# Kernel tuning notes

Hardware: AMD Instinct MI355X
Metric: run time of the kernel (lower is better)

Reference implementation:

```python
import jax, jax.numpy as jnp
import numpy as np

NUM_FEATURES = 4
LATENT = 16
HIDDEN = 128
N_PIECES = 20
B, P = 8192, 128


def setup_inputs() -> dict:
    key = jax.random.key(0)
    ks = jax.random.split(key, 8)
    s = lambda fan_in: 1.0 / np.sqrt(fan_in)
    return {
        "x": jax.random.normal(ks[0], (B, P * NUM_FEATURES), jnp.float32),
        "W1": jax.random.normal(ks[1], (NUM_FEATURES, HIDDEN), jnp.float32) * s(NUM_FEATURES),
        "b1": jnp.zeros((HIDDEN,), jnp.float32),
        "W2": jax.random.normal(ks[2], (HIDDEN, HIDDEN), jnp.float32) * s(HIDDEN),
        "b2": jnp.zeros((HIDDEN,), jnp.float32),
        "W3": jax.random.normal(ks[3], (HIDDEN, 2 * LATENT), jnp.float32) * s(HIDDEN),
        "b3": jnp.zeros((2 * LATENT,), jnp.float32),
        "pool_weight": jax.random.normal(ks[4], (2 * LATENT, N_PIECES + 1), jnp.float32) * 0.1,
        "eps": jax.random.normal(ks[5], (B, LATENT), jnp.float32),
    }


def _fspool_weights(pool_weight, set_size):
    # piecewise-linear interpolation of pool_weight over normalized rank positions
    pos = jnp.arange(set_size, dtype=jnp.float32) / (set_size - 1) * N_PIECES  # [P]
    idx = jnp.clip(pos.astype(jnp.int32), 0, N_PIECES)
    frac = pos - idx.astype(jnp.float32)
    left = pool_weight[:, idx]                                   # [C, P]
    right = pool_weight[:, jnp.clip(idx + 1, 0, N_PIECES)]       # [C, P]
    return (1.0 - frac) * left + frac * right                    # [C, P]


def reference(x, W1, b1, W2, b2, W3, b3, pool_weight, eps):
    # per-particle shared MLP, batched over particles (B, P, F) -> (B, P, 2L)
    h = x.reshape(B, P, NUM_FEATURES)
    h = jax.nn.relu(jnp.einsum("bpf,fh->bph", h, W1) + b1)
    h = jax.nn.relu(jnp.einsum("bph,hk->bpk", h, W2) + b2)
    h = jnp.einsum("bph,hc->bpc", h, W3) + b3                    # [B, P, 2L]
    z = jnp.transpose(h, (0, 2, 1))                              # [B, 2L, P]
    # FSPool: descending featurewise sort + rank-weighted sum over set dim
    z_sorted = jnp.flip(jnp.sort(z, axis=-1), axis=-1)           # [B, 2L, P]
    w = _fspool_weights(pool_weight, P)                          # [2L, P]
    pooled = jnp.sum(z_sorted * w[None], axis=-1)                # [B, 2L]
    mus = pooled[:, ::2]
    logvars = pooled[:, 1::2]
    samples = mus + eps * jnp.exp(0.5 * logvars)
    return (mus, logvars, samples)
```

## Files before the change

### kernel.cpp

```cpp
#include <hip/hip_runtime.h>

#define B_TOT 8192
#define NB    16
#define NPCS  20

typedef __attribute__((ext_vector_type(8))) __fp16 f16x8;
typedef __attribute__((ext_vector_type(4))) float f32x4;
typedef __attribute__((ext_vector_type(2))) __fp16 fp16x2;

__device__ __forceinline__ unsigned pkmax(unsigned a, unsigned b) {
    unsigned d; asm("v_pk_max_f16 %0, %1, %2" : "=v"(d) : "v"(a), "v"(b)); return d;
}
__device__ __forceinline__ unsigned pkmin(unsigned a, unsigned b) {
    unsigned d; asm("v_pk_min_f16 %0, %1, %2" : "=v"(d) : "v"(a), "v"(b)); return d;
}
__device__ __forceinline__ unsigned pkrne(float a, float b) {
    fp16x2 h;
    h.x = (__fp16)a;
    h.y = (__fp16)b;
    return __builtin_bit_cast(unsigned, h);
}
__device__ __forceinline__ unsigned pkrtz(float a, float b) {
    return __builtin_bit_cast(unsigned, __builtin_amdgcn_cvt_pkrtz(a, b));
}
__device__ __forceinline__ float asf(unsigned u) { return __builtin_bit_cast(float, u); }
__device__ __forceinline__ unsigned asu(float f) { return __builtin_bit_cast(unsigned, f); }
__device__ __forceinline__ fp16x2 ash2(unsigned u) { return __builtin_bit_cast(fp16x2, u); }
__device__ __forceinline__ unsigned asu2(fp16x2 h) { return __builtin_bit_cast(unsigned, h); }

template<int CTRL>
__device__ __forceinline__ unsigned dppmov(unsigned v) {
    return (unsigned)__builtin_amdgcn_mov_dpp((int)v, CTRL, 0xf, 0xf, true);
}
__device__ __forceinline__ unsigned xlane(unsigned v, int lm) {
    switch (lm) {
    case 1:  return dppmov<0xB1>(v);
    case 2:  return dppmov<0x4E>(v);
    case 4:  return (unsigned)__builtin_amdgcn_ds_swizzle((int)v, 0x101F);
    default: return dppmov<0x128>(v);
    }
}
__device__ __forceinline__ float xlanef(float v, int lm) { return asf(xlane(asu(v), lm)); }

#define WS_W3T 32768
#define WS_WSP 40960
#define WS_W1D 57344
#define WS_B1D 59392

__device__ __forceinline__ unsigned dup16(float f) {
    unsigned short u = __builtin_bit_cast(unsigned short, (__fp16)f);
    return (unsigned)u * 0x10001u;
}

__device__ __forceinline__ int piperm(int j) {
    return (j & 0x60) | ((j & 0x0C) << 1) | ((j & 0x10) >> 2) | (j & 3);
}

__global__ void prep_kernel(const float* __restrict__ W1, const float* __restrict__ b1,
                            const float* __restrict__ W2, const float* __restrict__ W3,
                            const float* __restrict__ pw, void* __restrict__ ws)
{
    const int t = blockIdx.x * 256 + threadIdx.x;
    __fp16* w2t = (__fp16*)ws;
    __fp16* w3t = (__fp16*)((char*)ws + WS_W3T);
    float* wsp  = (float*)((char*)ws + WS_WSP);
    unsigned* w1d = (unsigned*)((char*)ws + WS_W1D);
    unsigned* b1d = (unsigned*)((char*)ws + WS_B1D);
    if (t < 16384) {
        int j = t >> 7, k = t & 127;
        w2t[t] = (__fp16)W2[k * 128 + piperm(j)];
    } else if (t < 20480) {
        int o = t - 16384, c = o >> 7, k = o & 127;
        w3t[o] = (__fp16)W3[k * 32 + c];
    } else if (t < 24576) {
        int o = t - 20480, c = o >> 7, p = o & 127;
        float pos = (float)p * (20.0f / 127.0f);
        int ip = min((int)pos, NPCS);
        float fr = pos - (float)ip;
        int ipb = min(ip + 1, NPCS);
        wsp[o] = (1.0f - fr) * pw[c * 21 + ip] + fr * pw[c * 21 + ipb];
    } else if (t < 24704) {
        int h = t - 24576;
        w1d[h * 4 + 0] = dup16(W1[h]);
        w1d[h * 4 + 1] = dup16(W1[128 + h]);
        w1d[h * 4 + 2] = dup16(W1[256 + h]);
        w1d[h * 4 + 3] = dup16(W1[384 + h]);
        b1d[h] = dup16(b1[h]);
    }
}

#define L_SZP  32768
#define L_W1D  41216
#define L_B1D  43264
#define L_POOL 43776

__global__ __launch_bounds__(256, 2) void enc_kernel(
    const float* __restrict__ x,   const float* __restrict__ b1g,
    const float* __restrict__ b2g, const float* __restrict__ b3g,
    const float* __restrict__ eps, const void* __restrict__ ws,
    float* __restrict__ out)
{
    __shared__ __align__(16) char smem[45824];

    const int tid  = threadIdx.x;
    const int wv   = tid >> 6;
    const int lane = tid & 63;
    const int l16  = lane & 15;
    const int quad = lane >> 4;
    const int b0   = blockIdx.x * NB;

    {
        const uint4* src = (const uint4*)ws;
#pragma unroll
        for (int it = 0; it < 8; ++it) {
            int idx = tid + it * 256;
            int j = idx >> 4, ch = idx & 15;
            *(uint4*)(smem + j * 256 + ((ch ^ (j & 15)) * 16)) = src[idx];
        }
    }
    if (tid < 160) ((uint4*)(smem + L_W1D))[tid] = ((const uint4*)((const char*)ws + WS_W1D))[tid];

    f16x8 w3f[2][4];
    {
        const __fp16* w3t = (const __fp16*)((const char*)ws + WS_W3T);
#pragma unroll
        for (int mt2 = 0; mt2 < 2; ++mt2)
#pragma unroll
            for (int kt = 0; kt < 4; ++kt)
                w3f[mt2][kt] = *(const f16x8*)(w3t + (mt2 * 16 + l16) * 128 + kt * 32 + quad * 8);
    }
    f32x4 b3acc[2];
    {
        float4 t0 = *(const float4*)(b3g + quad * 4);
        float4 t1 = *(const float4*)(b3g + 16 + quad * 4);
        b3acc[0] = (f32x4){t0.x, t0.y, t0.z, t0.w};
        b3acc[1] = (f32x4){t1.x, t1.y, t1.z, t1.w};
    }
    f32x4 b2acc[8];
#pragma unroll
    for (int nt = 0; nt < 8; ++nt) {
        float4 t4 = *(const float4*)(b2g + (nt >> 1) * 32 + quad * 8 + (nt & 1) * 4);
        b2acc[nt] = (f32x4){t4.x, t4.y, t4.z, t4.w};
    }

    const int pr = wv * 4 + quad;
    float wE[8], wO[8];
    {
        const float* wsp = (const float*)((const char*)ws + WS_WSP);
        float4 e0 = *(const float4*)(wsp + (2 * pr) * 128 + l16 * 8);
        float4 e1 = *(const float4*)(wsp + (2 * pr) * 128 + l16 * 8 + 4);
        float4 o0 = *(const float4*)(wsp + (2 * pr + 1) * 128 + l16 * 8);
        float4 o1 = *(const float4*)(wsp + (2 * pr + 1) * 128 + l16 * 8 + 4);
        wE[0]=e0.x; wE[1]=e0.y; wE[2]=e0.z; wE[3]=e0.w; wE[4]=e1.x; wE[5]=e1.y; wE[6]=e1.z; wE[7]=e1.w;
        wO[0]=o0.x; wO[1]=o0.y; wO[2]=o0.z; wO[3]=o0.w; wO[4]=o1.x; wO[5]=o1.y; wO[6]=o1.z; wO[7]=o1.w;
    }

    const int ib = l16 * 8;
    const unsigned sfl8  = (ib & 8)  ? 0x80008000u : 0u;
    const unsigned sfl16 = (ib & 16) ? 0x80008000u : 0u;
    const unsigned sfl32 = (ib & 32) ? 0x80008000u : 0u;
    const unsigned sfl64 = (ib & 64) ? 0x80008000u : 0u;

    __syncthreads();

    unsigned* szp   = (unsigned*)(smem + L_SZP);
    float*    spool = (float*)(smem + L_POOL);

    const float* xptr = x + (size_t)b0 * 512 + (wv * 32 + l16) * 4;
    float4 xv0 = *(const float4*)(xptr);
    float4 xv1 = *(const float4*)(xptr + 64);

    for (int e = 0; e < NB; ++e) {
        const unsigned xp0 = pkrtz(xv0.x, xv1.x);
        const unsigned xp1 = pkrtz(xv0.y, xv1.y);
        const unsigned xp2 = pkrtz(xv0.z, xv1.z);
        const unsigned xp3 = pkrtz(xv0.w, xv1.w);

        if (e + 1 < NB) {
            xv0 = *(const float4*)(xptr + (e + 1) * 512);
            xv1 = *(const float4*)(xptr + (e + 1) * 512 + 64);
        }

        union AF { unsigned u[4]; f16x8 v; } a1[2][4];
#pragma unroll
        for (int kt = 0; kt < 4; ++kt) {
            const int k8 = kt * 32 + quad * 8;
#pragma unroll
            for (int jp = 0; jp < 4; ++jp) {
                const int h = k8 + 2 * jp;
                const uint4 wa = *(const uint4*)(smem + L_W1D + h * 16);
                const uint4 wb = *(const uint4*)(smem + L_W1D + h * 16 + 16);
                const uint2 bp = *(const uint2*)(smem + L_B1D + h * 4);
                fp16x2 accA = ash2(bp.x);
                fp16x2 accB = ash2(bp.y);
                accA = __builtin_elementwise_fma(ash2(xp0), ash2(wa.x), accA);
                accA = __builtin_elementwise_fma(ash2(xp1), ash2(wa.y), accA);
                accA = __builtin_elementwise_fma(ash2(xp2), ash2(wa.z), accA);
                accA = __builtin_elementwise_fma(ash2(xp3), ash2(wa.w), accA);
                accB = __builtin_elementwise_fma(ash2(xp0), ash2(wb.x), accB);
                accB = __builtin_elementwise_fma(ash2(xp1), ash2(wb.y), accB);
                accB = __builtin_elementwise_fma(ash2(xp2), ash2(wb.z), accB);
                accB = __builtin_elementwise_fma(ash2(xp3), ash2(wb.w), accB);
                const unsigned uA = pkmax(asu2(accA), 0u);
                const unsigned uB = pkmax(asu2(accB), 0u);
                a1[0][kt].u[jp] = __builtin_amdgcn_perm(uA, uB, 0x01000504u);
                a1[1][kt].u[jp] = __builtin_amdgcn_perm(uA, uB, 0x03020706u);
            }
        }

        f32x4 acc2[2][8];
#pragma unroll
        for (int kt = 0; kt < 4; ++kt)
#pragma unroll
            for (int nt = 0; nt < 8; ++nt) {
                const int j = nt * 16 + l16;
                const int phys = (kt * 4 + quad) ^ l16;
                f16x8 wf = *(const f16x8*)(smem + j * 256 + phys * 16);
                if (kt == 0) {
                    acc2[0][nt] = __builtin_amdgcn_mfma_f32_16x16x32_f16(wf, a1[0][0].v, b2acc[nt], 0, 0, 0);
                    acc2[1][nt] = __builtin_amdgcn_mfma_f32_16x16x32_f16(wf, a1[1][0].v, b2acc[nt], 0, 0, 0);
                } else {
                    acc2[0][nt] = __builtin_amdgcn_mfma_f32_16x16x32_f16(wf, a1[0][kt].v, acc2[0][nt], 0, 0, 0);
                    acc2[1][nt] = __builtin_amdgcn_mfma_f32_16x16x32_f16(wf, a1[1][kt].v, acc2[1][nt], 0, 0, 0);
                }
            }

#pragma unroll
        for (int mt = 0; mt < 2; ++mt) {
            unsigned pkx[8], pky[8];
#pragma unroll
            for (int nt = 0; nt < 8; ++nt) {
                pkx[nt] = pkmax(pkrtz(acc2[mt][nt][0], acc2[mt][nt][1]), 0u);
                pky[nt] = pkmax(pkrtz(acc2[mt][nt][2], acc2[mt][nt][3]), 0u);
            }
            union A3 { unsigned u[4]; f16x8 v; } a3[4];
#pragma unroll
            for (int kt = 0; kt < 4; ++kt) {
                a3[kt].u[0] = pkx[2 * kt];
                a3[kt].u[1] = pky[2 * kt];
                a3[kt].u[2] = pkx[2 * kt + 1];
                a3[kt].u[3] = pky[2 * kt + 1];
            }

            const int colbase = wv * 32 + mt * 16;
#pragma unroll
            for (int mt2 = 0; mt2 < 2; ++mt2) {
                f32x4 acc = __builtin_amdgcn_mfma_f32_16x16x32_f16(w3f[mt2][0], a3[0].v, b3acc[mt2], 0, 0, 0);
#pragma unroll
                for (int kt = 1; kt < 4; ++kt)
                    acc = __builtin_amdgcn_mfma_f32_16x16x32_f16(w3f[mt2][kt], a3[kt].v, acc, 0, 0, 0);
                const int prw = 8 * mt2 + 2 * quad;
                szp[prw * 132 + colbase + l16]       = pkrne(acc[0], acc[1]);
                szp[(prw + 1) * 132 + colbase + l16] = pkrne(acc[2], acc[3]);
            }
        }
        __syncthreads();

        unsigned v[8];
        {
            const unsigned* zp = szp + pr * 132 + l16 * 8;
            uint4 za = *(const uint4*)zp;
            uint4 zb = *(const uint4*)(zp + 4);
            v[0]=za.x; v[1]=za.y; v[2]=za.z; v[3]=za.w;
            v[4]=zb.x; v[5]=zb.y; v[6]=zb.z; v[7]=zb.w;
        }
#pragma unroll
        for (int k = 2; k <= 128; k <<= 1) {
#pragma unroll
            for (int j = 64; j >= 1; j >>= 1) {
                if (j >= k) continue;
                if (j >= 8) {
                    const bool km = ((ib & k) == 0) != ((ib & j) != 0);
                    const int lm = j >> 3;
#pragma unroll
                    for (int r = 0; r < 8; ++r) {
                        unsigned p = xlane(v[r], lm);
                        unsigned mx = pkmax(v[r], p), mn = pkmin(v[r], p);
                        v[r] = km ? mx : mn;
                    }
                } else if (k <= 4) {
#pragma unroll
                    for (int a = 0; a < 8; ++a) {
                        if (a & j) continue;
                        const int bx = a | j;
                        unsigned mx = pkmax(v[a], v[bx]), mn = pkmin(v[a], v[bx]);
                        if ((a & k) == 0) { v[a] = mx; v[bx] = mn; }
                        else              { v[a] = mn; v[bx] = mx; }
                    }
                } else {
                    const unsigned sfl = (k == 8) ? sfl8 : (k == 16) ? sfl16 :
                                         (k == 32) ? sfl32 : (k == 64) ? sfl64 : 0u;
                    if (j == 4 && k != 128) {
#pragma unroll
                        for (int r = 0; r < 8; ++r) v[r] ^= sfl;
                    }
#pragma unroll
                    for (int a = 0; a < 8; ++a) {
                        if (a & j) continue;
                        const int bx = a | j;
                        unsigned mx = pkmax(v[a], v[bx]), mn = pkmin(v[a], v[bx]);
                        v[a] = mx; v[bx] = mn;
                    }
                    if (j == 1 && k != 128) {
#pragma unroll
                        for (int r = 0; r < 8; ++r) v[r] ^= sfl;
                    }
                }
            }
        }

        float sE = 0.f, sO = 0.f;
#pragma unroll
        for (int r = 0; r < 8; ++r) {
            const fp16x2 hv = ash2(v[r]);
            sE = fmaf(wE[r], (float)hv.x, sE);
            sO = fmaf(wO[r], (float)hv.y, sO);
        }
#pragma unroll
        for (int d = 8; d >= 1; d >>= 1) {
            sE += xlanef(sE, d);
            sO += xlanef(sO, d);
        }
        if (l16 == 0) {
            spool[e * 32 + 2 * pr]     = sE;
            spool[e * 32 + 2 * pr + 1] = sO;
        }
        __syncthreads();
    }

    {
        const int e = tid >> 4, t = tid & 15;
        const float mu = spool[e * 32 + 2 * t];
        const float lv = spool[e * 32 + 2 * t + 1];
        const float ev = eps[(size_t)b0 * 16 + tid];
        const float smp = fmaf(ev, __expf(0.5f * lv), mu);
        out[(size_t)b0 * 16 + tid] = mu;
        out[(size_t)B_TOT * 16 + (size_t)b0 * 16 + tid] = lv;
        out[(size_t)2 * B_TOT * 16 + (size_t)b0 * 16 + tid] = smp;
    }
}

extern "C" void kernel_launch(void* const* d_in, const int* in_sizes, int n_in,
                              void* d_out, int out_size, void* d_ws, size_t ws_size,
                              hipStream_t stream) {
    const float* x   = (const float*)d_in[0];
    const float* W1  = (const float*)d_in[1];
    const float* b1  = (const float*)d_in[2];
    const float* W2  = (const float*)d_in[3];
    const float* b2  = (const float*)d_in[4];
    const float* W3  = (const float*)d_in[5];
    const float* b3  = (const float*)d_in[6];
    const float* pw  = (const float*)d_in[7];
    const float* eps = (const float*)d_in[8];
    float* out = (float*)d_out;

    prep_kernel<<<dim3(97), dim3(256), 0, stream>>>(W1, b1, W2, W3, pw, d_ws);
    enc_kernel<<<dim3(B_TOT / NB), dim3(256), 0, stream>>>(x, b1, b2, b3, eps, d_ws, out);
}
```

Measured before the change: 157.6 us.

## Compute first MLP layer with MFMA instead of packed fp16 FMAs

Replaces the per-lane packed-half FMA evaluation of layer 1 (4 inputs to 128 hidden) with 16x16x32 MFMA ops. W1 and b1 are prepacked into register-resident A fragments, with the bias folded in through a constant-one input column. This removes the W1/b1 LDS tables and their per-iteration shared-memory reads and VALU FMAs. In exchange it spends 16 MFMAs per element on mostly zero-padded K, plus extra fp32-to-fp16 conversions and more registers for the W1 fragments.

```diff
diff --git a/kernel.cpp b/kernel.cpp
--- a/kernel.cpp
+++ b/kernel.cpp
@@ -44,12 +44,13 @@
 
 #define WS_W3T 32768
 #define WS_WSP 40960
-#define WS_W1D 57344
-#define WS_B1D 59392
-
-__device__ __forceinline__ unsigned dup16(float f) {
-    unsigned short u = __builtin_bit_cast(unsigned short, (__fp16)f);
-    return (unsigned)u * 0x10001u;
+#define WS_W1A 57344
+#define WS_B1F 61440
+
+__device__ __forceinline__ unsigned packh2(float lo, float hi) {
+    unsigned short a = __builtin_bit_cast(unsigned short, (__fp16)lo);
+    unsigned short b = __builtin_bit_cast(unsigned short, (__fp16)hi);
+    return (unsigned)a | ((unsigned)b << 16);
 }
 
 __device__ __forceinline__ int piperm(int j) {
@@ -64,8 +65,8 @@
     __fp16* w2t = (__fp16*)ws;
     __fp16* w3t = (__fp16*)((char*)ws + WS_W3T);
     float* wsp  = (float*)((char*)ws + WS_WSP);
-    unsigned* w1d = (unsigned*)((char*)ws + WS_W1D);
-    unsigned* b1d = (unsigned*)((char*)ws + WS_B1D);
+    unsigned* w1a = (unsigned*)((char*)ws + WS_W1A);
+    unsigned* b1f = (unsigned*)((char*)ws + WS_B1F);
     if (t < 16384) {
         int j = t >> 7, k = t & 127;
         w2t[t] = (__fp16)W2[k * 128 + piperm(j)];
@@ -79,20 +80,31 @@
         float fr = pos - (float)ip;
         int ipb = min(ip + 1, NPCS);
         wsp[o] = (1.0f - fr) * pw[c * 21 + ip] + fr * pw[c * 21 + ipb];
-    } else if (t < 24704) {
-        int h = t - 24576;
-        w1d[h * 4 + 0] = dup16(W1[h]);
-        w1d[h * 4 + 1] = dup16(W1[128 + h]);
-        w1d[h * 4 + 2] = dup16(W1[256 + h]);
-        w1d[h * 4 + 3] = dup16(W1[384 + h]);
-        b1d[h] = dup16(b1[h]);
+    } else if (t < 25600) {
+        int idx = t - 24576;
+        int ht = idx >> 7, lane = (idx >> 1) & 63, pair = idx & 1;
+        int quad = lane >> 4, l16 = lane & 15;
+        unsigned val = 0;
+        if (quad == 0) {
+            int sh = piperm(16 * ht + l16);
+            val = packh2(W1[(2 * pair) * 128 + sh], W1[(2 * pair + 1) * 128 + sh]);
+        }
+        w1a[idx] = val;
+    } else if (t < 26112) {
+        int idx = t - 25600;
+        int ht = idx >> 6, lane = idx & 63;
+        int quad = lane >> 4, l16 = lane & 15;
+        unsigned val = 0;
+        if (quad == 0) {
+            int sh = piperm(16 * ht + l16);
+            val = packh2(b1[sh], 0.0f);
+        }
+        b1f[idx] = val;
     }
 }
 
 #define L_SZP  32768
-#define L_W1D  41216
-#define L_B1D  43264
-#define L_POOL 43776
+#define L_POOL 41216
 
 __global__ __launch_bounds__(256, 2) void enc_kernel(
     const float* __restrict__ x,   const float* __restrict__ b1g,
@@ -100,7 +112,7 @@
     const float* __restrict__ eps, const void* __restrict__ ws,
     float* __restrict__ out)
 {
-    __shared__ __align__(16) char smem[45824];
+    __shared__ __align__(16) char smem[43264];
 
     const int tid  = threadIdx.x;
     const int wv   = tid >> 6;
@@ -118,7 +130,6 @@
             *(uint4*)(smem + j * 256 + ((ch ^ (j & 15)) * 16)) = src[idx];
         }
     }
-    if (tid < 160) ((uint4*)(smem + L_W1D))[tid] = ((const uint4*)((const char*)ws + WS_W1D))[tid];
 
     f16x8 w3f[2][4];
     {
@@ -128,6 +139,19 @@
 #pragma unroll
             for (int kt = 0; kt < 4; ++kt)
                 w3f[mt2][kt] = *(const f16x8*)(w3t + (mt2 * 16 + l16) * 128 + kt * 32 + quad * 8);
+    }
+    union WF { unsigned u[4]; f16x8 v; } w1f[8];
+    {
+        const unsigned* w1a = (const unsigned*)((const char*)ws + WS_W1A);
+        const unsigned* b1f = (const unsigned*)((const char*)ws + WS_B1F);
+#pragma unroll
+        for (int ht = 0; ht < 8; ++ht) {
+            uint2 w01 = *(const uint2*)(w1a + ht * 128 + lane * 2);
+            w1f[ht].u[0] = w01.x;
+            w1f[ht].u[1] = w01.y;
+            w1f[ht].u[2] = b1f[ht * 64 + lane];
+            w1f[ht].u[3] = 0;
+        }
     }
     f32x4 b3acc[2];
     {
@@ -166,15 +190,20 @@
     unsigned* szp   = (unsigned*)(smem + L_SZP);
     float*    spool = (float*)(smem + L_POOL);
 
+    union XB { unsigned u[4]; f16x8 v; } xb0, xb1;
+    xb0.u[2] = 0x3C003C00u; xb0.u[3] = 0;
+    xb1.u[2] = 0x3C003C00u; xb1.u[3] = 0;
+    const f32x4 zc = (f32x4){0.f, 0.f, 0.f, 0.f};
+
     const float* xptr = x + (size_t)b0 * 512 + (wv * 32 + l16) * 4;
     float4 xv0 = *(const float4*)(xptr);
     float4 xv1 = *(const float4*)(xptr + 64);
 
     for (int e = 0; e < NB; ++e) {
-        const unsigned xp0 = pkrtz(xv0.x, xv1.x);
-        const unsigned xp1 = pkrtz(xv0.y, xv1.y);
-        const unsigned xp2 = pkrtz(xv0.z, xv1.z);
-        const unsigned xp3 = pkrtz(xv0.w, xv1.w);
+        xb0.u[0] = pkrtz(xv0.x, xv0.y);
+        xb0.u[1] = pkrtz(xv0.z, xv0.w);
+        xb1.u[0] = pkrtz(xv1.x, xv1.y);
+        xb1.u[1] = pkrtz(xv1.z, xv1.w);
 
         if (e + 1 < NB) {
             xv0 = *(const float4*)(xptr + (e + 1) * 512);
@@ -183,29 +212,14 @@
 
         union AF { unsigned u[4]; f16x8 v; } a1[2][4];
 #pragma unroll
-        for (int kt = 0; kt < 4; ++kt) {
-            const int k8 = kt * 32 + quad * 8;
-#pragma unroll
-            for (int jp = 0; jp < 4; ++jp) {
-                const int h = k8 + 2 * jp;
-                const uint4 wa = *(const uint4*)(smem + L_W1D + h * 16);
-                const uint4 wb = *(const uint4*)(smem + L_W1D + h * 16 + 16);
-                const uint2 bp = *(const uint2*)(smem + L_B1D + h * 4);
-                fp16x2 accA = ash2(bp.x);
-                fp16x2 accB = ash2(bp.y);
-                accA = __builtin_elementwise_fma(ash2(xp0), ash2(wa.x), accA);
-                accA = __builtin_elementwise_fma(ash2(xp1), ash2(wa.y), accA);
-                accA = __builtin_elementwise_fma(ash2(xp2), ash2(wa.z), accA);
-                accA = __builtin_elementwise_fma(ash2(xp3), ash2(wa.w), accA);
-                accB = __builtin_elementwise_fma(ash2(xp0), ash2(wb.x), accB);
-                accB = __builtin_elementwise_fma(ash2(xp1), ash2(wb.y), accB);
-                accB = __builtin_elementwise_fma(ash2(xp2), ash2(wb.z), accB);
-                accB = __builtin_elementwise_fma(ash2(xp3), ash2(wb.w), accB);
-                const unsigned uA = pkmax(asu2(accA), 0u);
-                const unsigned uB = pkmax(asu2(accB), 0u);
-                a1[0][kt].u[jp] = __builtin_amdgcn_perm(uA, uB, 0x01000504u);
-                a1[1][kt].u[jp] = __builtin_amdgcn_perm(uA, uB, 0x03020706u);
-            }
+        for (int ht = 0; ht < 8; ++ht) {
+            f32x4 d0 = __builtin_amdgcn_mfma_f32_16x16x32_f16(w1f[ht].v, xb0.v, zc, 0, 0, 0);
+            f32x4 d1 = __builtin_amdgcn_mfma_f32_16x16x32_f16(w1f[ht].v, xb1.v, zc, 0, 0, 0);
+            const int kt = ht >> 1, jb = 2 * (ht & 1);
+            a1[0][kt].u[jb]     = pkmax(pkrtz(d0[0], d0[1]), 0u);
+            a1[0][kt].u[jb + 1] = pkmax(pkrtz(d0[2], d0[3]), 0u);
+            a1[1][kt].u[jb]     = pkmax(pkrtz(d1[0], d1[1]), 0u);
+            a1[1][kt].u[jb + 1] = pkmax(pkrtz(d1[2], d1[3]), 0u);
         }
 
         f32x4 acc2[2][8];
@@ -354,6 +368,6 @@
     const float* eps = (const float*)d_in[8];
     float* out = (float*)d_out;
 
-    prep_kernel<<<dim3(97), dim3(256), 0, stream>>>(W1, b1, W2, W3, pw, d_ws);
+    prep_kernel<<<dim3(102), dim3(256), 0, stream>>>(W1, b1, W2, W3, pw, d_ws);
     enc_kernel<<<dim3(B_TOT / NB), dim3(256), 0, stream>>>(x, b1, b2, b3, eps, d_ws, out);
 }
```

Result: faster. 144.9 us (-8.0%).
